# Performance work log

Measured on AMD Instinct MI355X. Metric: run time of the kernel, lower is better.

## Reference

```python
import jax, jax.numpy as jnp
import numpy as np

NEG_INF = -1e9  # module uses -1e9 negativeInfinity constant
BS, DA, SL, H = 16, 512, 1024, 8


def setup_inputs() -> dict:
    key = jax.random.key(0)
    ks = jax.random.split(key, 8)
    return {
        "q":    jax.random.normal(ks[0], (BS, DA, SL), dtype=jnp.float32),
        "k_in": jax.random.normal(ks[1], (BS, DA, SL), dtype=jnp.float32),
        "v_in": jax.random.normal(ks[2], (BS, DA, SL), dtype=jnp.float32),
        "k_w":  jax.random.normal(ks[3], (DA, DA), dtype=jnp.float32) * 0.05,
        "k_b":  jax.random.normal(ks[4], (DA,), dtype=jnp.float32) * 0.05,
        "v_w":  jax.random.normal(ks[5], (DA, DA), dtype=jnp.float32) * 0.05,
        "v_b":  jax.random.normal(ks[6], (DA,), dtype=jnp.float32) * 0.05,
        "gbn_gamma": jnp.ones((H,), dtype=jnp.float32),
        "gbn_bias":  jnp.zeros((H,), dtype=jnp.float32),
        "gbn_m":     jnp.zeros((H,), dtype=jnp.float32),
        "gbn_s":     jnp.ones((H,), dtype=jnp.float32),
        "mask": jax.random.randint(ks[7], (BS, 1, 1, SL), 0, 2, dtype=jnp.int32),
    }


def reference(q, k_in, v_in, k_w, k_b, v_w, v_b, gbn_gamma, gbn_bias, gbn_m, gbn_s, mask):
    bs, da, qsl = q.shape
    h = gbn_gamma.shape[0]
    dh = da // h
    sl = k_in.shape[2]
    mask_b = mask.astype(bool)                 # [bs,1,1,sl] True = masked

    # 1x1 conv1d projections == per-position matmul over channels
    k = jnp.einsum('ok,bks->bos', k_w, k_in) + k_b[None, :, None]   # [bs,da,sl]
    v = jnp.einsum('ov,bvs->bos', v_w, v_in) + v_b[None, :, None]   # [bs,dva,sl]
    dva = v.shape[1]
    dvh = dva // h

    qh = q.reshape(bs, h, dh, qsl).transpose(0, 1, 3, 2)   # [bs,h,qsl,dh]
    kh = k.reshape(bs, h, dh, sl)                          # [bs,h,dh,sl]
    vh = v.reshape(bs, h, dvh, sl).transpose(0, 1, 3, 2)   # [bs,h,sl,dvh]

    scores = jnp.einsum('bhqd,bhds->bhqs', qh, kh)         # [bs,h,qsl,sl]

    # GhostBatchNorm1d(features=h) in eval mode: per-head affine normalization
    scores = (scores - gbn_m[None, :, None, None]) / gbn_s[None, :, None, None]
    scores = scores * gbn_gamma[None, :, None, None] + gbn_bias[None, :, None, None]

    mask_k = mask_b                           # [bs,1,1,sl]  mask key positions (selfAttention fill)
    mask_q = jnp.swapaxes(mask_b, 2, 3)       # [bs,1,sl,1]  mask query rows (transposed fill)
    scores = jnp.where(mask_k, NEG_INF, scores)
    scores = jnp.where(mask_q, NEG_INF, scores)

    w = jax.nn.softmax(scores, axis=-1)
    w = jnp.where(mask_q, 0.0, w)             # v_weights.masked_fill(mask, 0)

    out = jnp.einsum('bhqs,bhsd->bhqd', w, vh)             # [bs,h,qsl,dvh]
    out = out.transpose(0, 1, 3, 2).reshape(bs, dva, qsl)  # back to channels-first
    return out
```

## Files before the change

### kernel.cpp

```cpp
#include <hip/hip_runtime.h>

typedef _Float16 f16;
typedef _Float16 h8_t __attribute__((ext_vector_type(8)));
typedef _Float16 h4_t __attribute__((ext_vector_type(4)));
typedef float f32x4 __attribute__((ext_vector_type(4)));
typedef float f32x16 __attribute__((ext_vector_type(16)));

#define BS 16
#define DA 512
#define SL 1024
#define NH 8
#define DH 64

__device__ __forceinline__ void gload_lds16(const void* g, void* l) {
  __builtin_amdgcn_global_load_lds((const __attribute__((address_space(1))) void*)g,
                                   (__attribute__((address_space(3))) void*)l, 16, 0, 0);
}

__global__ __launch_bounds__(256) void prep_kernel(
    const float* __restrict__ k_in, const float* __restrict__ v_in,
    const float* __restrict__ k_w, const float* __restrict__ v_w,
    f16* __restrict__ Kt, f16* __restrict__ Vt,
    f16* __restrict__ kwh, f16* __restrict__ vwh) {
  const int blk = blockIdx.x;
  const int t = threadIdx.x;
  if (blk < 2048) {
    const int which = blk >> 10;
    const int r = blk & 1023;
    const int b = r >> 6;
    const int c0 = ((r >> 3) & 7) * 64;
    const int s0 = (r & 7) * 128;
    const float* src = which ? v_in : k_in;
    f16* dst = which ? Vt : Kt;
    __shared__ __align__(16) float Xf32[64 * 132];
#pragma unroll
    for (int p = 0; p < 8; ++p) {
      const int idx = p * 256 + t;
      const int cc = idx >> 5, s4 = (idx & 31) * 4;
      const float4 v = *(const float4*)&src[((size_t)b * DA + c0 + cc) * SL + s0 + s4];
      *(float4*)&Xf32[cc * 132 + s4] = v;
    }
    __syncthreads();
    const int srow = t >> 1, cb = (t & 1) * 32;
#pragma unroll
    for (int g = 0; g < 4; ++g) {
      h8_t h;
#pragma unroll
      for (int u = 0; u < 8; ++u) h[u] = (f16)Xf32[(cb + g * 8 + u) * 132 + srow];
      *(h8_t*)&dst[((size_t)b * SL + s0 + srow) * DA + c0 + cb + g * 8] = h;
    }
  } else {
    const int r = blk - 2048;
    const int wsel = r >> 5;
    const float* src = wsel ? v_w : k_w;
    f16* dst = wsel ? vwh : kwh;
    const int base = (r & 31) * 8192;
#pragma unroll
    for (int p = 0; p < 4; ++p) {
      const int i = base + p * 2048 + t * 8;
      const float4 a = *(const float4*)&src[i];
      const float4 c = *(const float4*)&src[i + 4];
      h8_t h;
      h[0] = (f16)a.x; h[1] = (f16)a.y; h[2] = (f16)a.z; h[3] = (f16)a.w;
      h[4] = (f16)c.x; h[5] = (f16)c.y; h[6] = (f16)c.z; h[7] = (f16)c.w;
      *(h8_t*)&dst[i] = h;
    }
  }
}

template <int MODE>
__global__ __launch_bounds__(256) void proj_gemm(const f16* __restrict__ Ag,
                                                 const f16* __restrict__ Bg,
                                                 const float* __restrict__ bias,
                                                 f16* __restrict__ outg) {
  constexpr int MT = MODE ? SL : DA;
  constexpr int NT = MODE ? DA : SL;
  __shared__ __align__(16) f16 Al[128 * 32];
  __shared__ __align__(16) f16 Bl[128 * 32];
  const int b = blockIdx.z;
  const int m0 = blockIdx.x * 128, n0 = blockIdx.y * 128;
  const int t = threadIdx.x;
  const int lane = t & 63, w = t >> 6, lr = lane & 15, lq = lane >> 4;
  const int wm = (w >> 1) * 64, wn = (w & 1) * 64;

  const f16* Arow = Ag + (MODE ? (size_t)b * SL * DA : 0) + (size_t)m0 * DA;
  const f16* Brow = Bg + (MODE ? 0 : (size_t)b * SL * DA) + (size_t)n0 * DA;

  const int rr = t >> 2;
  const int c8 = (t & 3) * 8;

  f32x4 acc[4][4] = {};

  for (int kt = 0; kt < 16; ++kt) {
    const int c0 = kt * 32;
    __syncthreads();
    gload_lds16(Arow + (size_t)rr * DA + c0 + c8, Al + t * 8);
    gload_lds16(Arow + (size_t)(64 + rr) * DA + c0 + c8, Al + 2048 + t * 8);
    gload_lds16(Brow + (size_t)rr * DA + c0 + c8, Bl + t * 8);
    gload_lds16(Brow + (size_t)(64 + rr) * DA + c0 + c8, Bl + 2048 + t * 8);
    __syncthreads();
    h8_t af[4], bf[4];
#pragma unroll
    for (int i = 0; i < 4; ++i) af[i] = *(const h8_t*)&Al[(wm + i * 16 + lr) * 32 + lq * 8];
#pragma unroll
    for (int j = 0; j < 4; ++j) bf[j] = *(const h8_t*)&Bl[(wn + j * 16 + lr) * 32 + lq * 8];
#pragma unroll
    for (int i = 0; i < 4; ++i)
#pragma unroll
      for (int j = 0; j < 4; ++j)
        acc[i][j] = __builtin_amdgcn_mfma_f32_16x16x32_f16(af[i], bf[j], acc[i][j], 0, 0, 0);
  }

#pragma unroll
  for (int i = 0; i < 4; ++i) {
    const int gmb = m0 + wm + i * 16 + lq * 4;
    float bm[4] = {0.f, 0.f, 0.f, 0.f};
    if (MODE == 0) {
      const float4 b4 = *(const float4*)&bias[gmb];
      bm[0] = b4.x; bm[1] = b4.y; bm[2] = b4.z; bm[3] = b4.w;
    }
#pragma unroll
    for (int j = 0; j < 4; ++j) {
      const int gn = n0 + wn + j * 16 + lr;
      const float bn = (MODE == 1) ? bias[gn] : 0.f;
      h4_t hv;
#pragma unroll
      for (int r = 0; r < 4; ++r) {
        const float val = acc[i][j][r] + (MODE == 0 ? bm[r] : bn);
        hv[r] = (f16)val;
      }
      *(h4_t*)&outg[((size_t)b * NT + gn) * MT + gmb] = hv;
    }
  }
}

template <int MODE>
__global__ __launch_bounds__(256) void fused_proj(const float* __restrict__ Wg,
                                                  const float* __restrict__ Xin,
                                                  const float* __restrict__ bias,
                                                  f16* __restrict__ outg) {
  constexpr int MT = MODE ? SL : DA;
  constexpr int NT = MODE ? DA : SL;
  __shared__ f16 Wl[128 * 40];
  __shared__ f16 Xl[128 * 40];
  __shared__ float Xf32[32 * 132];
  const int b = blockIdx.z;
  const int m0 = blockIdx.x * 128;
  const int n0 = blockIdx.y * 128;
  const int o_base = MODE ? n0 : m0;
  const int s_base = MODE ? m0 : n0;
  const int t = threadIdx.x;
  const int w = t >> 6, lane = t & 63, lr = lane & 15, lq = lane >> 4;
  const int wm = (w >> 1) * 64, wn = (w & 1) * 64;

  f32x4 acc[4][4] = {};

  for (int kt = 0; kt < 16; ++kt) {
    const int c0 = kt * 32;
    __syncthreads();
#pragma unroll
    for (int p = 0; p < 4; ++p) {
      const int idx = p * 256 + t;
      const int row = idx >> 3, cq = (idx & 7) * 4;
      const float4 v = *(const float4*)&Wg[(size_t)(o_base + row) * DA + c0 + cq];
      h4_t hv;
      hv[0] = (f16)v.x; hv[1] = (f16)v.y; hv[2] = (f16)v.z; hv[3] = (f16)v.w;
      *(h4_t*)&Wl[row * 40 + cq] = hv;
    }
#pragma unroll
    for (int p = 0; p < 4; ++p) {
      const int idx = p * 256 + t;
      const int cc = idx >> 5, s4 = (idx & 31) * 4;
      const float4 v = *(const float4*)&Xin[((size_t)b * DA + c0 + cc) * SL + s_base + s4];
      *(float4*)&Xf32[cc * 132 + s4] = v;
    }
    __syncthreads();
    {
      const int srow = t >> 1, cb = (t & 1) * 16;
      h8_t lo, hi;
#pragma unroll
      for (int u = 0; u < 8; ++u) lo[u] = (f16)Xf32[(cb + u) * 132 + srow];
#pragma unroll
      for (int u = 0; u < 8; ++u) hi[u] = (f16)Xf32[(cb + 8 + u) * 132 + srow];
      *(h8_t*)&Xl[srow * 40 + cb] = lo;
      *(h8_t*)&Xl[srow * 40 + cb + 8] = hi;
    }
    __syncthreads();
    const f16* Alp = MODE ? Xl : Wl;
    const f16* Blp = MODE ? Wl : Xl;
    h8_t af[4], bf[4];
#pragma unroll
    for (int i = 0; i < 4; ++i) af[i] = *(const h8_t*)&Alp[(wm + i * 16 + lr) * 40 + lq * 8];
#pragma unroll
    for (int j = 0; j < 4; ++j) bf[j] = *(const h8_t*)&Blp[(wn + j * 16 + lr) * 40 + lq * 8];
#pragma unroll
    for (int i = 0; i < 4; ++i)
#pragma unroll
      for (int j = 0; j < 4; ++j)
        acc[i][j] = __builtin_amdgcn_mfma_f32_16x16x32_f16(af[i], bf[j], acc[i][j], 0, 0, 0);
  }

#pragma unroll
  for (int i = 0; i < 4; ++i) {
    const int gmb = m0 + wm + i * 16 + lq * 4;
    float bm[4] = {0.f, 0.f, 0.f, 0.f};
    if (MODE == 0) {
      const float4 b4 = *(const float4*)&bias[gmb];
      bm[0] = b4.x; bm[1] = b4.y; bm[2] = b4.z; bm[3] = b4.w;
    }
#pragma unroll
    for (int j = 0; j < 4; ++j) {
      const int gn = n0 + wn + j * 16 + lr;
      const float bn = (MODE == 1) ? bias[gn] : 0.f;
      h4_t hv;
#pragma unroll
      for (int r = 0; r < 4; ++r) {
        const float val = acc[i][j][r] + (MODE == 0 ? bm[r] : bn);
        hv[r] = (f16)val;
      }
      *(h4_t*)&outg[((size_t)b * NT + gn) * MT + gmb] = hv;
    }
  }
}

__global__ __launch_bounds__(256, 2) void attn_kernel(
    const float* __restrict__ qg, const f16* __restrict__ kp, const f16* __restrict__ vp,
    const float* __restrict__ gamma, const float* __restrict__ gbns,
    const int* __restrict__ maskg, float* __restrict__ outg) {
  __shared__ __align__(16) char smem[36864];
  f16* KV = (f16*)smem;
  float* Osh = (float*)smem;

  const int bh = blockIdx.x, b = bh >> 3, h = bh & 7;
  const int i0 = blockIdx.y * 256;
  const int t = threadIdx.x, w = t >> 6, lane = t & 63;
  const int l5 = lane & 31, hf = lane >> 5;
  const float scale = gamma[h] / gbns[h] * 1.44269504088896f;

  h8_t qf[2][4];
#pragma unroll
  for (int im = 0; im < 2; ++im)
#pragma unroll
    for (int ks = 0; ks < 4; ++ks) {
      h8_t v;
#pragma unroll
      for (int u = 0; u < 8; ++u) {
        const int d = ks * 16 + hf * 8 + u;
        v[u] = (f16)(qg[((size_t)b * DA + h * DH + d) * SL + i0 + w * 64 + im * 32 + l5] * scale);
      }
      qf[im][ks] = v;
    }

  const int srow = t >> 3;
  const int c8 = (t & 7) * 8;

  uint4 rk[2], rv[2];
#pragma unroll
  for (int p = 0; p < 2; ++p) {
    const int row = p * 32 + srow;
    rk[p] = *(const uint4*)&kp[((size_t)b * SL + row) * DA + h * DH + c8];
    rv[p] = *(const uint4*)&vp[((size_t)b * DA + h * DH + row) * SL + c8];
  }
  {
    f16* K0 = KV;
    f16* V0 = KV + 4608;
#pragma unroll
    for (int p = 0; p < 2; ++p) {
      const int row = p * 32 + srow;
      const int rowp = (row & ~12) | ((row & 4) << 1) | ((row & 8) >> 1);
      *(uint4*)&K0[rowp * 72 + c8] = rk[p];
      *(uint4*)&V0[row * 72 + c8] = rv[p];
    }
  }
  __syncthreads();

  float m_i[2] = {-3e38f, -3e38f}, l_i[2] = {0.f, 0.f};
  f32x16 acc[2][2] = {};

  for (int jt = 0; jt < 16; ++jt) {
    const int j0 = jt * 64;
    const f16* Kc = KV + (jt & 1) * 9216;
    const f16* Vc = Kc + 4608;

    if (jt < 15) {
      const int jn = j0 + 64;
#pragma unroll
      for (int p = 0; p < 2; ++p) {
        const int row = p * 32 + srow;
        rk[p] = *(const uint4*)&kp[((size_t)b * SL + jn + row) * DA + h * DH + c8];
        rv[p] = *(const uint4*)&vp[((size_t)b * DA + h * DH + row) * SL + jn + c8];
      }
    }
    int4 mq[2][4];
#pragma unroll
    for (int mj = 0; mj < 2; ++mj)
#pragma unroll
      for (int q = 0; q < 4; ++q)
        mq[mj][q] = *(const int4*)&maskg[b * SL + j0 + mj * 32 + (q >> 1) * 16 + hf * 8 + (q & 1) * 4];

    f32x16 sa[2][2] = {};
#pragma unroll
    for (int ks = 0; ks < 4; ++ks)
#pragma unroll
      for (int mj = 0; mj < 2; ++mj) {
        const h8_t kf = *(const h8_t*)&Kc[(mj * 32 + l5) * 72 + ks * 16 + hf * 8];
#pragma unroll
        for (int im = 0; im < 2; ++im)
          sa[im][mj] = __builtin_amdgcn_mfma_f32_32x32x16_f16(kf, qf[im][ks], sa[im][mj], 0, 0, 0);
      }

#pragma unroll
    for (int mj = 0; mj < 2; ++mj)
#pragma unroll
      for (int q = 0; q < 4; ++q) {
        const int4 m4 = mq[mj][q];
#pragma unroll
        for (int im = 0; im < 2; ++im) {
          if (m4.x) sa[im][mj][q * 4 + 0] = -1e9f;
          if (m4.y) sa[im][mj][q * 4 + 1] = -1e9f;
          if (m4.z) sa[im][mj][q * 4 + 2] = -1e9f;
          if (m4.w) sa[im][mj][q * 4 + 3] = -1e9f;
        }
      }

    float alpha[2];
#pragma unroll
    for (int im = 0; im < 2; ++im) {
      float mx = sa[im][0][0];
#pragma unroll
      for (int e = 1; e < 16; ++e) mx = fmaxf(mx, sa[im][0][e]);
#pragma unroll
      for (int e = 0; e < 16; ++e) mx = fmaxf(mx, sa[im][1][e]);
      mx = fmaxf(mx, __shfl_xor(mx, 32));
      const float mn = fmaxf(m_i[im], mx);
      alpha[im] = __builtin_amdgcn_exp2f(m_i[im] - mn);
      m_i[im] = mn;
      float rs = 0.f;
#pragma unroll
      for (int mj = 0; mj < 2; ++mj)
#pragma unroll
        for (int e = 0; e < 16; ++e) {
          const float pv = __builtin_amdgcn_exp2f(sa[im][mj][e] - mn);
          sa[im][mj][e] = pv;
          rs += pv;
        }
      rs += __shfl_xor(rs, 32);
      l_i[im] = l_i[im] * alpha[im] + rs;
#pragma unroll
      for (int nd = 0; nd < 2; ++nd)
#pragma unroll
        for (int e = 0; e < 16; ++e) acc[im][nd][e] *= alpha[im];
    }

#pragma unroll
    for (int jk = 0; jk < 4; ++jk) {
      const int mj = jk >> 1, g = jk & 1;
      h8_t pf[2];
#pragma unroll
      for (int im = 0; im < 2; ++im) {
        h8_t pk;
#pragma unroll
        for (int u = 0; u < 8; ++u) pk[u] = (f16)sa[im][mj][g * 8 + u];
        pf[im] = pk;
      }
#pragma unroll
      for (int nd = 0; nd < 2; ++nd) {
        const h8_t vf = *(const h8_t*)&Vc[(nd * 32 + l5) * 72 + jk * 16 + hf * 8];
#pragma unroll
        for (int im = 0; im < 2; ++im)
          acc[im][nd] = __builtin_amdgcn_mfma_f32_32x32x16_f16(vf, pf[im], acc[im][nd], 0, 0, 0);
      }
    }

    if (jt < 15) {
      f16* Kn = KV + ((jt + 1) & 1) * 9216;
      f16* Vn = Kn + 4608;
#pragma unroll
      for (int p = 0; p < 2; ++p) {
        const int row = p * 32 + srow;
        const int rowp = (row & ~12) | ((row & 4) << 1) | ((row & 8) >> 1);
        *(uint4*)&Kn[rowp * 72 + c8] = rk[p];
        *(uint4*)&Vn[row * 72 + c8] = rv[p];
      }
      __syncthreads();
    }
  }

  float fac[2];
#pragma unroll
  for (int im = 0; im < 2; ++im) {
    const int mo = maskg[b * SL + i0 + w * 64 + im * 32 + l5];
    fac[im] = mo ? 0.f : 1.f / l_i[im];
  }
  __syncthreads();

#pragma unroll
  for (int nd = 0; nd < 2; ++nd) {
#pragma unroll
    for (int im = 0; im < 2; ++im)
#pragma unroll
      for (int e = 0; e < 16; ++e) {
        const int dl = (e & 3) + 8 * (e >> 2) + 4 * hf;
        Osh[dl * 256 + w * 64 + im * 32 + l5] = acc[im][nd][e] * fac[im];
      }
    __syncthreads();
#pragma unroll
    for (int pass = 0; pass < 8; ++pass) {
      const int row = pass * 4 + w;
      const int i4 = lane * 4;
      const float4 o = *(const float4*)&Osh[row * 256 + i4];
      *(float4*)&outg[((size_t)b * DA + h * DH + nd * 32 + row) * SL + i0 + i4] = o;
    }
    __syncthreads();
  }
}

extern "C" void kernel_launch(void* const* d_in, const int* in_sizes, int n_in,
                              void* d_out, int out_size, void* d_ws, size_t ws_size,
                              hipStream_t stream) {
  const float* q     = (const float*)d_in[0];
  const float* k_in  = (const float*)d_in[1];
  const float* v_in  = (const float*)d_in[2];
  const float* k_w   = (const float*)d_in[3];
  const float* k_b   = (const float*)d_in[4];
  const float* v_w   = (const float*)d_in[5];
  const float* v_b   = (const float*)d_in[6];
  const float* gamma = (const float*)d_in[7];
  const float* gbns  = (const float*)d_in[10];
  const int*   mask  = (const int*)d_in[11];
  float* out = (float*)d_out;

  const size_t NEL = (size_t)BS * SL * DA;
  f16* kpw = (f16*)d_ws;
  f16* vpw = kpw + NEL;

  const size_t need = NEL * 2 * 4 + (size_t)DA * DA * 2 * 2;
  if (ws_size >= need) {
    f16* Kt  = vpw + NEL;
    f16* Vt  = Kt + NEL;
    f16* kwh = Vt + NEL;
    f16* vwh = kwh + (size_t)DA * DA;
    prep_kernel<<<dim3(2112), 256, 0, stream>>>(k_in, v_in, k_w, v_w, Kt, Vt, kwh, vwh);
    proj_gemm<0><<<dim3(4, 8, BS), 256, 0, stream>>>(kwh, Kt, k_b, kpw);
    proj_gemm<1><<<dim3(8, 4, BS), 256, 0, stream>>>(Vt, vwh, v_b, vpw);
  } else {
    fused_proj<0><<<dim3(4, 8, BS), 256, 0, stream>>>(k_w, k_in, k_b, kpw);
    fused_proj<1><<<dim3(8, 4, BS), 256, 0, stream>>>(v_w, v_in, v_b, vpw);
  }
  attn_kernel<<<dim3(BS * NH, SL / 256), 256, 0, stream>>>(q, kpw, vpw, gamma, gbns, mask, out);
}
```

Before: 255.9 us.

## Merge K/V projection GEMMs, double-buffer LDS, shrink attention query tile, lazy rescale

The two projection GEMMs become a single launch, and that kernel double-buffers its LDS tiles so the next k-slice loads while MFMAs run on the current one. The attention kernel now gives each wave 32 query rows instead of 64, doubling the grid and raising launch_bounds occupancy to 4 blocks per CU. It also skips the online-softmax rescale unless the running max grows by more than 8, and adds setprio hints around the MFMA sections. The trade-off is that K/V tiles get reloaded for twice as many blocks, and the lazy rescale lets exp2 values reach up to 2^8 before normalisation, which adds some fp16 rounding risk.

```diff
diff --git a/kernel.cpp b/kernel.cpp
--- a/kernel.cpp
+++ b/kernel.cpp
@@ -68,68 +68,90 @@
   }
 }
 
-template <int MODE>
-__global__ __launch_bounds__(256) void proj_gemm(const f16* __restrict__ Ag,
-                                                 const f16* __restrict__ Bg,
-                                                 const float* __restrict__ bias,
-                                                 f16* __restrict__ outg) {
-  constexpr int MT = MODE ? SL : DA;
-  constexpr int NT = MODE ? DA : SL;
-  __shared__ __align__(16) f16 Al[128 * 32];
-  __shared__ __align__(16) f16 Bl[128 * 32];
-  const int b = blockIdx.z;
-  const int m0 = blockIdx.x * 128, n0 = blockIdx.y * 128;
+__global__ __launch_bounds__(256, 4) void proj_gemm_all(
+    const f16* __restrict__ kwh, const f16* __restrict__ vwh,
+    const f16* __restrict__ Kt, const f16* __restrict__ Vt,
+    const float* __restrict__ k_b, const float* __restrict__ v_b,
+    f16* __restrict__ kp, f16* __restrict__ vp) {
+  __shared__ __align__(16) f16 LD[2][8192];
+  const int mode = blockIdx.z;
+  const int b = blockIdx.y;
+  const int tx = blockIdx.x;
+  const int m0 = (mode ? (tx >> 2) : (tx & 3)) * 128;
+  const int n0 = (mode ? (tx & 3) : (tx >> 2)) * 128;
   const int t = threadIdx.x;
   const int lane = t & 63, w = t >> 6, lr = lane & 15, lq = lane >> 4;
   const int wm = (w >> 1) * 64, wn = (w & 1) * 64;
 
-  const f16* Arow = Ag + (MODE ? (size_t)b * SL * DA : 0) + (size_t)m0 * DA;
-  const f16* Brow = Bg + (MODE ? 0 : (size_t)b * SL * DA) + (size_t)n0 * DA;
+  const f16* Arow = (mode ? Vt + (size_t)b * SL * DA : kwh) + (size_t)m0 * DA;
+  const f16* Brow = (mode ? vwh : Kt + (size_t)b * SL * DA) + (size_t)n0 * DA;
 
   const int rr = t >> 2;
   const int c8 = (t & 3) * 8;
+  const int lo8 = t * 8;
+
+  const f16* ga0 = Arow + (size_t)rr * DA + c8;
+  const f16* ga1 = Arow + (size_t)(64 + rr) * DA + c8;
+  const f16* gb0 = Brow + (size_t)rr * DA + c8;
+  const f16* gb1 = Brow + (size_t)(64 + rr) * DA + c8;
 
   f32x4 acc[4][4] = {};
 
+  gload_lds16(ga0, &LD[0][0] + lo8);
+  gload_lds16(ga1, &LD[0][2048] + lo8);
+  gload_lds16(gb0, &LD[0][4096] + lo8);
+  gload_lds16(gb1, &LD[0][6144] + lo8);
+  ga0 += 32; ga1 += 32; gb0 += 32; gb1 += 32;
+  __syncthreads();
+
   for (int kt = 0; kt < 16; ++kt) {
-    const int c0 = kt * 32;
-    __syncthreads();
-    gload_lds16(Arow + (size_t)rr * DA + c0 + c8, Al + t * 8);
-    gload_lds16(Arow + (size_t)(64 + rr) * DA + c0 + c8, Al + 2048 + t * 8);
-    gload_lds16(Brow + (size_t)rr * DA + c0 + c8, Bl + t * 8);
-    gload_lds16(Brow + (size_t)(64 + rr) * DA + c0 + c8, Bl + 2048 + t * 8);
-    __syncthreads();
+    const int cur = kt & 1;
+    if (kt < 15) {
+      f16* nb = &LD[cur ^ 1][0];
+      gload_lds16(ga0, nb + lo8);
+      gload_lds16(ga1, nb + 2048 + lo8);
+      gload_lds16(gb0, nb + 4096 + lo8);
+      gload_lds16(gb1, nb + 6144 + lo8);
+      ga0 += 32; ga1 += 32; gb0 += 32; gb1 += 32;
+    }
+    const f16* Al = &LD[cur][0];
+    const f16* Bl = &LD[cur][4096];
     h8_t af[4], bf[4];
 #pragma unroll
     for (int i = 0; i < 4; ++i) af[i] = *(const h8_t*)&Al[(wm + i * 16 + lr) * 32 + lq * 8];
 #pragma unroll
     for (int j = 0; j < 4; ++j) bf[j] = *(const h8_t*)&Bl[(wn + j * 16 + lr) * 32 + lq * 8];
+    __builtin_amdgcn_s_setprio(1);
 #pragma unroll
     for (int i = 0; i < 4; ++i)
 #pragma unroll
       for (int j = 0; j < 4; ++j)
         acc[i][j] = __builtin_amdgcn_mfma_f32_16x16x32_f16(af[i], bf[j], acc[i][j], 0, 0, 0);
+    __builtin_amdgcn_s_setprio(0);
+    __syncthreads();
   }
 
 #pragma unroll
   for (int i = 0; i < 4; ++i) {
     const int gmb = m0 + wm + i * 16 + lq * 4;
     float bm[4] = {0.f, 0.f, 0.f, 0.f};
-    if (MODE == 0) {
-      const float4 b4 = *(const float4*)&bias[gmb];
+    if (mode == 0) {
+      const float4 b4 = *(const float4*)&k_b[gmb];
       bm[0] = b4.x; bm[1] = b4.y; bm[2] = b4.z; bm[3] = b4.w;
     }
 #pragma unroll
     for (int j = 0; j < 4; ++j) {
       const int gn = n0 + wn + j * 16 + lr;
-      const float bn = (MODE == 1) ? bias[gn] : 0.f;
+      const float bn = mode ? v_b[gn] : 0.f;
       h4_t hv;
 #pragma unroll
       for (int r = 0; r < 4; ++r) {
-        const float val = acc[i][j][r] + (MODE == 0 ? bm[r] : bn);
+        const float val = acc[i][j][r] + (mode == 0 ? bm[r] : bn);
         hv[r] = (f16)val;
       }
-      *(h4_t*)&outg[((size_t)b * NT + gn) * MT + gmb] = hv;
+      f16* dst = mode ? &vp[((size_t)b * DA + gn) * SL + gmb]
+                      : &kp[((size_t)b * SL + gn) * DA + gmb];
+      *(h4_t*)dst = hv;
     }
   }
 }
@@ -223,7 +245,7 @@
   }
 }
 
-__global__ __launch_bounds__(256, 2) void attn_kernel(
+__global__ __launch_bounds__(256, 4) void attn_kernel(
     const float* __restrict__ qg, const f16* __restrict__ kp, const f16* __restrict__ vp,
     const float* __restrict__ gamma, const float* __restrict__ gbns,
     const int* __restrict__ maskg, float* __restrict__ outg) {
@@ -232,24 +254,23 @@
   float* Osh = (float*)smem;
 
   const int bh = blockIdx.x, b = bh >> 3, h = bh & 7;
-  const int i0 = blockIdx.y * 256;
+  const int i0 = blockIdx.y * 128;
   const int t = threadIdx.x, w = t >> 6, lane = t & 63;
   const int l5 = lane & 31, hf = lane >> 5;
   const float scale = gamma[h] / gbns[h] * 1.44269504088896f;
-
-  h8_t qf[2][4];
-#pragma unroll
-  for (int im = 0; im < 2; ++im)
-#pragma unroll
-    for (int ks = 0; ks < 4; ++ks) {
-      h8_t v;
-#pragma unroll
-      for (int u = 0; u < 8; ++u) {
-        const int d = ks * 16 + hf * 8 + u;
-        v[u] = (f16)(qg[((size_t)b * DA + h * DH + d) * SL + i0 + w * 64 + im * 32 + l5] * scale);
-      }
-      qf[im][ks] = v;
-    }
+  const int iw = i0 + w * 32 + l5;
+
+  h8_t qf[4];
+#pragma unroll
+  for (int ks = 0; ks < 4; ++ks) {
+    h8_t v;
+#pragma unroll
+    for (int u = 0; u < 8; ++u) {
+      const int d = ks * 16 + hf * 8 + u;
+      v[u] = (f16)(qg[((size_t)b * DA + h * DH + d) * SL + iw] * scale);
+    }
+    qf[ks] = v;
+  }
 
   const int srow = t >> 3;
   const int c8 = (t & 7) * 8;
@@ -274,8 +295,8 @@
   }
   __syncthreads();
 
-  float m_i[2] = {-3e38f, -3e38f}, l_i[2] = {0.f, 0.f};
-  f32x16 acc[2][2] = {};
+  float m_i = -3e38f, l_i = 0.f;
+  f32x16 acc[2] = {};
 
   for (int jt = 0; jt < 16; ++jt) {
     const int j0 = jt * 64;
@@ -298,79 +319,82 @@
       for (int q = 0; q < 4; ++q)
         mq[mj][q] = *(const int4*)&maskg[b * SL + j0 + mj * 32 + (q >> 1) * 16 + hf * 8 + (q & 1) * 4];
 
-    f32x16 sa[2][2] = {};
+    f32x16 sa[2] = {};
+    __builtin_amdgcn_s_setprio(1);
 #pragma unroll
     for (int ks = 0; ks < 4; ++ks)
 #pragma unroll
       for (int mj = 0; mj < 2; ++mj) {
         const h8_t kf = *(const h8_t*)&Kc[(mj * 32 + l5) * 72 + ks * 16 + hf * 8];
-#pragma unroll
-        for (int im = 0; im < 2; ++im)
-          sa[im][mj] = __builtin_amdgcn_mfma_f32_32x32x16_f16(kf, qf[im][ks], sa[im][mj], 0, 0, 0);
-      }
+        sa[mj] = __builtin_amdgcn_mfma_f32_32x32x16_f16(kf, qf[ks], sa[mj], 0, 0, 0);
+      }
+    __builtin_amdgcn_s_setprio(0);
 
 #pragma unroll
     for (int mj = 0; mj < 2; ++mj)
 #pragma unroll
       for (int q = 0; q < 4; ++q) {
         const int4 m4 = mq[mj][q];
-#pragma unroll
-        for (int im = 0; im < 2; ++im) {
-          if (m4.x) sa[im][mj][q * 4 + 0] = -1e9f;
-          if (m4.y) sa[im][mj][q * 4 + 1] = -1e9f;
-          if (m4.z) sa[im][mj][q * 4 + 2] = -1e9f;
-          if (m4.w) sa[im][mj][q * 4 + 3] = -1e9f;
+        if (m4.x) sa[mj][q * 4 + 0] = -1e9f;
+        if (m4.y) sa[mj][q * 4 + 1] = -1e9f;
+        if (m4.z) sa[mj][q * 4 + 2] = -1e9f;
+        if (m4.w) sa[mj][q * 4 + 3] = -1e9f;
+      }
+
+    float mx;
+    {
+      float a[8];
+#pragma unroll
+      for (int u = 0; u < 8; ++u)
+        a[u] = fmaxf(fmaxf(sa[0][u], sa[0][u + 8]), fmaxf(sa[1][u], sa[1][u + 8]));
+      const float b0 = fmaxf(a[0], a[1]), b1 = fmaxf(a[2], a[3]);
+      const float b2 = fmaxf(a[4], a[5]), b3 = fmaxf(a[6], a[7]);
+      mx = fmaxf(fmaxf(b0, b1), fmaxf(b2, b3));
+      mx = fmaxf(mx, __shfl_xor(mx, 32));
+    }
+    if (!__all(mx - m_i <= 8.0f)) {
+      const float mn = fmaxf(m_i, mx);
+      const float alpha = __builtin_amdgcn_exp2f(m_i - mn);
+      m_i = mn;
+      l_i *= alpha;
+#pragma unroll
+      for (int nd = 0; nd < 2; ++nd)
+#pragma unroll
+        for (int e = 0; e < 16; ++e) acc[nd][e] *= alpha;
+    }
+    {
+      float r0 = 0.f, r1 = 0.f, r2 = 0.f, r3 = 0.f;
+#pragma unroll
+      for (int mj = 0; mj < 2; ++mj)
+#pragma unroll
+        for (int e = 0; e < 16; e += 4) {
+          const float p0 = __builtin_amdgcn_exp2f(sa[mj][e + 0] - m_i);
+          const float p1 = __builtin_amdgcn_exp2f(sa[mj][e + 1] - m_i);
+          const float p2 = __builtin_amdgcn_exp2f(sa[mj][e + 2] - m_i);
+          const float p3 = __builtin_amdgcn_exp2f(sa[mj][e + 3] - m_i);
+          sa[mj][e + 0] = p0; sa[mj][e + 1] = p1;
+          sa[mj][e + 2] = p2; sa[mj][e + 3] = p3;
+          r0 += p0; r1 += p1; r2 += p2; r3 += p3;
         }
-      }
-
-    float alpha[2];
-#pragma unroll
-    for (int im = 0; im < 2; ++im) {
-      float mx = sa[im][0][0];
-#pragma unroll
-      for (int e = 1; e < 16; ++e) mx = fmaxf(mx, sa[im][0][e]);
-#pragma unroll
-      for (int e = 0; e < 16; ++e) mx = fmaxf(mx, sa[im][1][e]);
-      mx = fmaxf(mx, __shfl_xor(mx, 32));
-      const float mn = fmaxf(m_i[im], mx);
-      alpha[im] = __builtin_amdgcn_exp2f(m_i[im] - mn);
-      m_i[im] = mn;
-      float rs = 0.f;
-#pragma unroll
-      for (int mj = 0; mj < 2; ++mj)
-#pragma unroll
-        for (int e = 0; e < 16; ++e) {
-          const float pv = __builtin_amdgcn_exp2f(sa[im][mj][e] - mn);
-          sa[im][mj][e] = pv;
-          rs += pv;
-        }
+      float rs = (r0 + r1) + (r2 + r3);
       rs += __shfl_xor(rs, 32);
-      l_i[im] = l_i[im] * alpha[im] + rs;
-#pragma unroll
-      for (int nd = 0; nd < 2; ++nd)
-#pragma unroll
-        for (int e = 0; e < 16; ++e) acc[im][nd][e] *= alpha[im];
-    }
-
+      l_i += rs;
+    }
+
+    __builtin_amdgcn_s_setprio(1);
 #pragma unroll
     for (int jk = 0; jk < 4; ++jk) {
       const int mj = jk >> 1, g = jk & 1;
-      h8_t pf[2];
-#pragma unroll
-      for (int im = 0; im < 2; ++im) {
-        h8_t pk;
-#pragma unroll
-        for (int u = 0; u < 8; ++u) pk[u] = (f16)sa[im][mj][g * 8 + u];
-        pf[im] = pk;
-      }
+      h8_t pk;
+#pragma unroll
+      for (int u = 0; u < 8; ++u) pk[u] = (f16)sa[mj][g * 8 + u];
 #pragma unroll
       for (int nd = 0; nd < 2; ++nd) {
         const h8_t vf = *(const h8_t*)&Vc[(nd * 32 + l5) * 72 + jk * 16 + hf * 8];
-#pragma unroll
-        for (int im = 0; im < 2; ++im)
-          acc[im][nd] = __builtin_amdgcn_mfma_f32_32x32x16_f16(vf, pf[im], acc[im][nd], 0, 0, 0);
-      }
-    }
+        acc[nd] = __builtin_amdgcn_mfma_f32_32x32x16_f16(vf, pk, acc[nd], 0, 0, 0);
+      }
+    }
+    __builtin_amdgcn_s_setprio(0);
 
     if (jt < 15) {
       f16* Kn = KV + ((jt + 1) & 1) * 9216;
@@ -386,29 +410,23 @@
     }
   }
 
-  float fac[2];
-#pragma unroll
-  for (int im = 0; im < 2; ++im) {
-    const int mo = maskg[b * SL + i0 + w * 64 + im * 32 + l5];
-    fac[im] = mo ? 0.f : 1.f / l_i[im];
-  }
+  const int mo = maskg[b * SL + iw];
+  const float fac = mo ? 0.f : 1.f / l_i;
   __syncthreads();
 
 #pragma unroll
   for (int nd = 0; nd < 2; ++nd) {
 #pragma unroll
-    for (int im = 0; im < 2; ++im)
-#pragma unroll
-      for (int e = 0; e < 16; ++e) {
-        const int dl = (e & 3) + 8 * (e >> 2) + 4 * hf;
-        Osh[dl * 256 + w * 64 + im * 32 + l5] = acc[im][nd][e] * fac[im];
-      }
-    __syncthreads();
-#pragma unroll
-    for (int pass = 0; pass < 8; ++pass) {
-      const int row = pass * 4 + w;
-      const int i4 = lane * 4;
-      const float4 o = *(const float4*)&Osh[row * 256 + i4];
+    for (int e = 0; e < 16; ++e) {
+      const int dl = (e & 3) + 8 * (e >> 2) + 4 * hf;
+      Osh[dl * 128 + w * 32 + l5] = acc[nd][e] * fac;
+    }
+    __syncthreads();
+#pragma unroll
+    for (int pass = 0; pass < 4; ++pass) {
+      const int row = pass * 8 + (t >> 5);
+      const int i4 = (t & 31) * 4;
+      const float4 o = *(const float4*)&Osh[row * 128 + i4];
       *(float4*)&outg[((size_t)b * DA + h * DH + nd * 32 + row) * SL + i0 + i4] = o;
     }
     __syncthreads();
@@ -441,11 +459,10 @@
     f16* kwh = Vt + NEL;
     f16* vwh = kwh + (size_t)DA * DA;
     prep_kernel<<<dim3(2112), 256, 0, stream>>>(k_in, v_in, k_w, v_w, Kt, Vt, kwh, vwh);
-    proj_gemm<0><<<dim3(4, 8, BS), 256, 0, stream>>>(kwh, Kt, k_b, kpw);
-    proj_gemm<1><<<dim3(8, 4, BS), 256, 0, stream>>>(Vt, vwh, v_b, vpw);
+    proj_gemm_all<<<dim3(32, BS, 2), 256, 0, stream>>>(kwh, vwh, Kt, Vt, k_b, v_b, kpw, vpw);
   } else {
     fused_proj<0><<<dim3(4, 8, BS), 256, 0, stream>>>(k_w, k_in, k_b, kpw);
     fused_proj<1><<<dim3(8, 4, BS), 256, 0, stream>>>(v_w, v_in, v_b, vpw);
   }
-  attn_kernel<<<dim3(BS * NH, SL / 256), 256, 0, stream>>>(q, kpw, vpw, gamma, gbns, mask, out);
-}
+  attn_kernel<<<dim3(BS * NH, SL / 128), 256, 0, stream>>>(q, kpw, vpw, gamma, gbns, mask, out);
+}
```

Result: slower. 263.9 us (+3.1%).

## Merge K/V projection GEMMs and streamline attention softmax masking and rescaling

Applied to the files above, without the earlier changes.

Replaces the two projection GEMM launches with one kernel that handles both K and V via blockIdx.z. It stages 128x128 weight tiles in XOR-swizzled LDS and reads activation fragments straight from global memory. In attention, the per-tile int mask loads become a precomputed additive float bias held in LDS. The online softmax now skips the max update and accumulator rescale unless the new max exceeds the running max by more than 8 (lazy rescaling), and it uses tree reductions and s_setprio around the MFMA blocks. The goal is fewer launches and less per-tile VALU and memory work, at the cost of more LDS per block and uncached global fragment loads in the GEMM.

```diff
diff --git a/kernel.cpp b/kernel.cpp
--- a/kernel.cpp
+++ b/kernel.cpp
@@ -68,68 +68,101 @@
   }
 }
 
-template <int MODE>
-__global__ __launch_bounds__(256) void proj_gemm(const f16* __restrict__ Ag,
-                                                 const f16* __restrict__ Bg,
-                                                 const float* __restrict__ bias,
-                                                 f16* __restrict__ outg) {
-  constexpr int MT = MODE ? SL : DA;
-  constexpr int NT = MODE ? DA : SL;
-  __shared__ __align__(16) f16 Al[128 * 32];
-  __shared__ __align__(16) f16 Bl[128 * 32];
-  const int b = blockIdx.z;
-  const int m0 = blockIdx.x * 128, n0 = blockIdx.y * 128;
+__global__ __launch_bounds__(256, 4) void proj_gemm_all(
+    const f16* __restrict__ kwh, const f16* __restrict__ vwh,
+    const f16* __restrict__ Kt, const f16* __restrict__ Vt,
+    const float* __restrict__ k_b, const float* __restrict__ v_b,
+    f16* __restrict__ kp, f16* __restrict__ vp) {
+  __shared__ __align__(16) f16 Wl[128 * 128];
+  const int mode = blockIdx.z;
+  const int b = blockIdx.y;
+  const int tx = blockIdx.x;
+  const int ot = tx & 3, st = tx >> 2;
+  const int oo = ot * 128, ss = st * 128;
+  const int m0 = mode ? ss : oo;
+  const int n0 = mode ? oo : ss;
   const int t = threadIdx.x;
   const int lane = t & 63, w = t >> 6, lr = lane & 15, lq = lane >> 4;
   const int wm = (w >> 1) * 64, wn = (w & 1) * 64;
 
-  const f16* Arow = Ag + (MODE ? (size_t)b * SL * DA : 0) + (size_t)m0 * DA;
-  const f16* Brow = Bg + (MODE ? 0 : (size_t)b * SL * DA) + (size_t)n0 * DA;
-
-  const int rr = t >> 2;
-  const int c8 = (t & 3) * 8;
+  const f16* Wg = (mode ? vwh : kwh) + (size_t)oo * DA;
+  const f16* Xg = (mode ? Vt : Kt) + (size_t)b * SL * DA + (size_t)ss * DA;
+  const int xw = mode ? wm : wn;
+  const int ww = mode ? wn : wm;
 
   f32x4 acc[4][4] = {};
 
-  for (int kt = 0; kt < 16; ++kt) {
-    const int c0 = kt * 32;
-    __syncthreads();
-    gload_lds16(Arow + (size_t)rr * DA + c0 + c8, Al + t * 8);
-    gload_lds16(Arow + (size_t)(64 + rr) * DA + c0 + c8, Al + 2048 + t * 8);
-    gload_lds16(Brow + (size_t)rr * DA + c0 + c8, Bl + t * 8);
-    gload_lds16(Brow + (size_t)(64 + rr) * DA + c0 + c8, Bl + 2048 + t * 8);
-    __syncthreads();
-    h8_t af[4], bf[4];
-#pragma unroll
-    for (int i = 0; i < 4; ++i) af[i] = *(const h8_t*)&Al[(wm + i * 16 + lr) * 32 + lq * 8];
-#pragma unroll
-    for (int j = 0; j < 4; ++j) bf[j] = *(const h8_t*)&Bl[(wn + j * 16 + lr) * 32 + lq * 8];
-#pragma unroll
-    for (int i = 0; i < 4; ++i)
-#pragma unroll
-      for (int j = 0; j < 4; ++j)
-        acc[i][j] = __builtin_amdgcn_mfma_f32_16x16x32_f16(af[i], bf[j], acc[i][j], 0, 0, 0);
+#pragma unroll
+  for (int p = 0; p < 8; ++p) {
+    const int S = p * 4096 + t * 16;
+    const int u = (S ^ (((S >> 8) & 7) << 4)) >> 1;
+    gload_lds16(&Wg[(size_t)(u >> 7) * DA + (u & 127)], (char*)Wl + S);
+  }
+  __syncthreads();
+
+  for (int q = 0; q < 4; ++q) {
+    const int c0 = q * 128;
+#pragma unroll
+    for (int ks = 0; ks < 4; ++ks) {
+      h8_t xf[4], wf[4];
+#pragma unroll
+      for (int e = 0; e < 4; ++e) {
+        const int xrow = xw + e * 16 + lr;
+        xf[e] = *(const h8_t*)&Xg[(size_t)xrow * DA + c0 + ks * 32 + lq * 8];
+        const int wrow = ww + e * 16 + lr;
+        const int ba = (wrow << 8) + ks * 64 + lq * 16;
+        wf[e] = *(const h8_t*)((const char*)Wl + (ba ^ ((wrow & 7) << 4)));
+      }
+      __builtin_amdgcn_s_setprio(1);
+      if (mode == 0) {
+#pragma unroll
+        for (int i = 0; i < 4; ++i)
+#pragma unroll
+          for (int j = 0; j < 4; ++j)
+            acc[i][j] = __builtin_amdgcn_mfma_f32_16x16x32_f16(wf[i], xf[j], acc[i][j], 0, 0, 0);
+      } else {
+#pragma unroll
+        for (int i = 0; i < 4; ++i)
+#pragma unroll
+          for (int j = 0; j < 4; ++j)
+            acc[i][j] = __builtin_amdgcn_mfma_f32_16x16x32_f16(xf[i], wf[j], acc[i][j], 0, 0, 0);
+      }
+      __builtin_amdgcn_s_setprio(0);
+    }
+    if (q < 3) {
+      __syncthreads();
+      const int cn = (q + 1) * 128;
+#pragma unroll
+      for (int p = 0; p < 8; ++p) {
+        const int S = p * 4096 + t * 16;
+        const int u = (S ^ (((S >> 8) & 7) << 4)) >> 1;
+        gload_lds16(&Wg[(size_t)(u >> 7) * DA + cn + (u & 127)], (char*)Wl + S);
+      }
+      __syncthreads();
+    }
   }
 
 #pragma unroll
   for (int i = 0; i < 4; ++i) {
     const int gmb = m0 + wm + i * 16 + lq * 4;
     float bm[4] = {0.f, 0.f, 0.f, 0.f};
-    if (MODE == 0) {
-      const float4 b4 = *(const float4*)&bias[gmb];
+    if (mode == 0) {
+      const float4 b4 = *(const float4*)&k_b[gmb];
       bm[0] = b4.x; bm[1] = b4.y; bm[2] = b4.z; bm[3] = b4.w;
     }
 #pragma unroll
     for (int j = 0; j < 4; ++j) {
       const int gn = n0 + wn + j * 16 + lr;
-      const float bn = (MODE == 1) ? bias[gn] : 0.f;
+      const float bn = mode ? v_b[gn] : 0.f;
       h4_t hv;
 #pragma unroll
       for (int r = 0; r < 4; ++r) {
-        const float val = acc[i][j][r] + (MODE == 0 ? bm[r] : bn);
+        const float val = acc[i][j][r] + (mode == 0 ? bm[r] : bn);
         hv[r] = (f16)val;
       }
-      *(h4_t*)&outg[((size_t)b * NT + gn) * MT + gmb] = hv;
+      f16* dst = mode ? &vp[((size_t)b * DA + gn) * SL + gmb]
+                      : &kp[((size_t)b * SL + gn) * DA + gmb];
+      *(h4_t*)dst = hv;
     }
   }
 }
@@ -227,9 +260,10 @@
     const float* __restrict__ qg, const f16* __restrict__ kp, const f16* __restrict__ vp,
     const float* __restrict__ gamma, const float* __restrict__ gbns,
     const int* __restrict__ maskg, float* __restrict__ outg) {
-  __shared__ __align__(16) char smem[36864];
+  __shared__ __align__(16) char smem[36864 + 4096];
   f16* KV = (f16*)smem;
   float* Osh = (float*)smem;
+  float* biasf = (float*)(smem + 36864);
 
   const int bh = blockIdx.x, b = bh >> 3, h = bh & 7;
   const int i0 = blockIdx.y * 256;
@@ -251,6 +285,16 @@
       qf[im][ks] = v;
     }
 
+  {
+    const int4 m4 = *(const int4*)&maskg[b * SL + t * 4];
+    float4 b4;
+    b4.x = m4.x ? -1e9f : 0.f;
+    b4.y = m4.y ? -1e9f : 0.f;
+    b4.z = m4.z ? -1e9f : 0.f;
+    b4.w = m4.w ? -1e9f : 0.f;
+    *(float4*)&biasf[t * 4] = b4;
+  }
+
   const int srow = t >> 3;
   const int c8 = (t & 7) * 8;
 
@@ -291,14 +335,9 @@
         rv[p] = *(const uint4*)&vp[((size_t)b * DA + h * DH + row) * SL + jn + c8];
       }
     }
-    int4 mq[2][4];
-#pragma unroll
-    for (int mj = 0; mj < 2; ++mj)
-#pragma unroll
-      for (int q = 0; q < 4; ++q)
-        mq[mj][q] = *(const int4*)&maskg[b * SL + j0 + mj * 32 + (q >> 1) * 16 + hf * 8 + (q & 1) * 4];
 
     f32x16 sa[2][2] = {};
+    __builtin_amdgcn_s_setprio(1);
 #pragma unroll
     for (int ks = 0; ks < 4; ++ks)
 #pragma unroll
@@ -308,50 +347,61 @@
         for (int im = 0; im < 2; ++im)
           sa[im][mj] = __builtin_amdgcn_mfma_f32_32x32x16_f16(kf, qf[im][ks], sa[im][mj], 0, 0, 0);
       }
+    __builtin_amdgcn_s_setprio(0);
 
 #pragma unroll
     for (int mj = 0; mj < 2; ++mj)
 #pragma unroll
-      for (int q = 0; q < 4; ++q) {
-        const int4 m4 = mq[mj][q];
+      for (int qq = 0; qq < 4; ++qq) {
+        const float4 bq = *(const float4*)&biasf[j0 + mj * 32 + (qq >> 1) * 16 + hf * 8 + (qq & 1) * 4];
 #pragma unroll
         for (int im = 0; im < 2; ++im) {
-          if (m4.x) sa[im][mj][q * 4 + 0] = -1e9f;
-          if (m4.y) sa[im][mj][q * 4 + 1] = -1e9f;
-          if (m4.z) sa[im][mj][q * 4 + 2] = -1e9f;
-          if (m4.w) sa[im][mj][q * 4 + 3] = -1e9f;
+          sa[im][mj][qq * 4 + 0] += bq.x;
+          sa[im][mj][qq * 4 + 1] += bq.y;
+          sa[im][mj][qq * 4 + 2] += bq.z;
+          sa[im][mj][qq * 4 + 3] += bq.w;
         }
       }
 
-    float alpha[2];
 #pragma unroll
     for (int im = 0; im < 2; ++im) {
-      float mx = sa[im][0][0];
-#pragma unroll
-      for (int e = 1; e < 16; ++e) mx = fmaxf(mx, sa[im][0][e]);
-#pragma unroll
-      for (int e = 0; e < 16; ++e) mx = fmaxf(mx, sa[im][1][e]);
+      float a[8];
+#pragma unroll
+      for (int u = 0; u < 8; ++u)
+        a[u] = fmaxf(fmaxf(sa[im][0][u], sa[im][0][u + 8]),
+                     fmaxf(sa[im][1][u], sa[im][1][u + 8]));
+      float mx = fmaxf(fmaxf(fmaxf(a[0], a[1]), fmaxf(a[2], a[3])),
+                       fmaxf(fmaxf(a[4], a[5]), fmaxf(a[6], a[7])));
       mx = fmaxf(mx, __shfl_xor(mx, 32));
-      const float mn = fmaxf(m_i[im], mx);
-      alpha[im] = __builtin_amdgcn_exp2f(m_i[im] - mn);
-      m_i[im] = mn;
-      float rs = 0.f;
+      if (!__all(mx - m_i[im] <= 8.0f)) {
+        const float mn = fmaxf(m_i[im], mx);
+        const float alpha = __builtin_amdgcn_exp2f(m_i[im] - mn);
+        m_i[im] = mn;
+        l_i[im] *= alpha;
+#pragma unroll
+        for (int nd = 0; nd < 2; ++nd)
+#pragma unroll
+          for (int e = 0; e < 16; ++e) acc[im][nd][e] *= alpha;
+      }
+      float r0 = 0.f, r1 = 0.f, r2 = 0.f, r3 = 0.f;
 #pragma unroll
       for (int mj = 0; mj < 2; ++mj)
 #pragma unroll
-        for (int e = 0; e < 16; ++e) {
-          const float pv = __builtin_amdgcn_exp2f(sa[im][mj][e] - mn);
-          sa[im][mj][e] = pv;
-          rs += pv;
+        for (int e = 0; e < 16; e += 4) {
+          const float p0 = __builtin_amdgcn_exp2f(sa[im][mj][e + 0] - m_i[im]);
+          const float p1 = __builtin_amdgcn_exp2f(sa[im][mj][e + 1] - m_i[im]);
+          const float p2 = __builtin_amdgcn_exp2f(sa[im][mj][e + 2] - m_i[im]);
+          const float p3 = __builtin_amdgcn_exp2f(sa[im][mj][e + 3] - m_i[im]);
+          sa[im][mj][e + 0] = p0; sa[im][mj][e + 1] = p1;
+          sa[im][mj][e + 2] = p2; sa[im][mj][e + 3] = p3;
+          r0 += p0; r1 += p1; r2 += p2; r3 += p3;
         }
+      float rs = (r0 + r1) + (r2 + r3);
       rs += __shfl_xor(rs, 32);
-      l_i[im] = l_i[im] * alpha[im] + rs;
-#pragma unroll
-      for (int nd = 0; nd < 2; ++nd)
-#pragma unroll
-        for (int e = 0; e < 16; ++e) acc[im][nd][e] *= alpha[im];
-    }
-
+      l_i[im] += rs;
+    }
+
+    __builtin_amdgcn_s_setprio(1);
 #pragma unroll
     for (int jk = 0; jk < 4; ++jk) {
       const int mj = jk >> 1, g = jk & 1;
@@ -371,6 +421,7 @@
           acc[im][nd] = __builtin_amdgcn_mfma_f32_32x32x16_f16(vf, pf[im], acc[im][nd], 0, 0, 0);
       }
     }
+    __builtin_amdgcn_s_setprio(0);
 
     if (jt < 15) {
       f16* Kn = KV + ((jt + 1) & 1) * 9216;
@@ -441,8 +492,7 @@
     f16* kwh = Vt + NEL;
     f16* vwh = kwh + (size_t)DA * DA;
     prep_kernel<<<dim3(2112), 256, 0, stream>>>(k_in, v_in, k_w, v_w, Kt, Vt, kwh, vwh);
-    proj_gemm<0><<<dim3(4, 8, BS), 256, 0, stream>>>(kwh, Kt, k_b, kpw);
-    proj_gemm<1><<<dim3(8, 4, BS), 256, 0, stream>>>(Vt, vwh, v_b, vpw);
+    proj_gemm_all<<<dim3(32, BS, 2), 256, 0, stream>>>(kwh, vwh, Kt, Vt, k_b, v_b, kpw, vpw);
   } else {
     fused_proj<0><<<dim3(4, 8, BS), 256, 0, stream>>>(k_w, k_in, k_b, kpw);
     fused_proj<1><<<dim3(8, 4, BS), 256, 0, stream>>>(v_w, v_in, v_b, vpw);
```

New measurement: 390.7 us. +52.7%, slower.
